# Performance work log

Hardware: AMD Instinct MI355X
Metric: run time of the kernel (lower is better)

The kernel has to match this reference:

```python
import jax, jax.numpy as jnp
import numpy as np
import math


def _interp_linear(x, t_out):
    # x: [B, D, Lin] -> [B, D, t_out]; matches torch F.interpolate(mode='linear', align_corners=False)
    lin = x.shape[-1]
    pos = (jnp.arange(t_out, dtype=jnp.float32) + 0.5) * (lin / t_out) - 0.5
    pos = jnp.clip(pos, 0.0, lin - 1.0)
    lo = jnp.floor(pos).astype(jnp.int32)
    hi = jnp.minimum(lo + 1, lin - 1)
    w = pos - lo.astype(jnp.float32)
    return x[..., lo] * (1.0 - w) + x[..., hi] * w


def _forward(x, in_w, in_b, gq_w, gq_b, gk_w, gk_b, gv_w, gv_b, go_w, go_b, curv,
             wav0, wav1, wav2, wav3, wrec_w, wrec_b,
             te1_w, te1_b, te2_w, te2_b, td1_w, td1_b, td2_w, td2_b, bd_w, bd_b,
             cc_w, cc_b, ln_g, ln_b, mm1_w, mm1_b, mm2_w, mm2_b,
             dn1_w, dn1_b, dn2_w, dn2_b, dn3_w, dn3_b, out_w, out_b,
             noise_sched, noise):
    B, T, _ = x.shape
    L, H = curv.shape
    D = in_w.shape[1]
    hd = D // H
    dn = ('NCH', 'OIH', 'NCH')
    h = x @ in_w + in_b
    total_loss = jnp.float32(0.0)
    wavs = [wav0, wav1, wav2, wav3]
    for l in range(L):  # static small layer loop
        # ---- GeometricAttention (vectorized hyperbolic-distance softmax) ----
        q = (h @ gq_w[l] + gq_b[l]).reshape(B, T, H, hd)
        k = (h @ gk_w[l] + gk_b[l]).reshape(B, T, H, hd)
        v = (h @ gv_w[l] + gv_b[l]).reshape(B, T, H, hd)
        c = jnp.abs(curv[l]) + 1e-8                       # [H]
        cb = c[None, :, None, None]
        qn = jnp.einsum('bthd,bthd->bht', q, q)           # [B,H,T]
        kn = jnp.einsum('bthd,bthd->bht', k, k)
        qk = jnp.einsum('bihd,bjhd->bhij', q, k)          # [B,H,T,T]
        d2 = jnp.maximum(qn[:, :, :, None] + kn[:, :, None, :] - 2.0 * qk, 0.0)
        denom = jnp.maximum((1.0 - cb * qn[:, :, :, None]) * (1.0 - cb * kn[:, :, None, :]), 1e-5)
        arg = jnp.maximum(1.0 + cb * (2.0 * d2) / denom, 1.00001)
        dist = jnp.arccosh(arg) / jnp.sqrt(cb)
        attn = jax.nn.softmax(-dist, axis=-1)             # temperature = 1.0
        geom = jnp.einsum('bhij,bjhd->bihd', attn, v).reshape(B, T, D) @ go_w[l] + go_b[l]
        # ---- WaveletTransform ----
        xf = h.transpose(0, 2, 1)                          # [B,D,T]
        decomps = []
        for i, wv in enumerate(wavs):
            filt = jax.nn.softmax(wv[l], axis=-1)          # [D,K]
            K = filt.shape[-1]
            dec = jax.lax.conv_general_dilated(xf, filt[:, None, :], (1,), [(K - 1, 0)],
                                               feature_group_count=D, dimension_numbers=dn)
            dec = dec[:, :, ::2 ** (i + 1)]
            decomps.append(_interp_linear(dec, T))
        comb = jnp.concatenate(decomps, axis=1).transpose(0, 2, 1)  # [B,T,4D]
        wave = comb @ wrec_w[l] + wrec_b[l]
        # ---- TopologicalLayer ----
        tf = jax.nn.relu(h @ te1_w[l] + te1_b[l]) @ te2_w[l] + te2_b[l]
        topo = h + (jax.nn.relu(tf @ td1_w[l] + td1_b[l]) @ td2_w[l] + td2_b[l])
        bd = tf @ bd_w[l] + bd_b[l]
        total_loss = total_loss + jnp.mean(jax.nn.relu(bd[..., 0] - bd[..., 1] + 0.1))
        # ---- CausalConvolution (kernel 3, dilation 2**l) ----
        dil = 2 ** l
        pad = 2 * dil
        cc = jax.lax.conv_general_dilated(h.transpose(0, 2, 1), cc_w[l], (1,), [(pad, 0)],
                                          rhs_dilation=(dil,), dimension_numbers=dn)
        cc = (cc + cc_b[l][None, :, None]).transpose(0, 2, 1)
        # ---- combine + LayerNorm (dropout is identity in eval) ----
        s = geom + wave + topo + cc
        mu = jnp.mean(s, axis=-1, keepdims=True)
        var = jnp.var(s, axis=-1, keepdims=True)
        h = (s - mu) / jnp.sqrt(var + 1e-5) * ln_g + ln_b
    # ---- manifold mixer (T > 1 branch) ----
    last = h[:, -1]
    pen = h[:, -2]
    mix = jnp.tanh(jnp.concatenate([last, pen], axis=-1) @ mm1_w + mm1_b) @ mm2_w + mm2_b
    cur = last + mix
    # ---- diffusion refinement ----
    half = D // 2
    emb_f = jnp.exp(jnp.arange(half, dtype=jnp.float32) * (-math.log(10000.0) / (half - 1)))
    S = noise.shape[0]
    for t in range(S):  # static diffusion_steps=10
        noisy = cur + noise[t] * noise_sched[t]
        te = jnp.full((B, 1), float(t), dtype=jnp.float32) * emb_f[None, :]
        temb = jnp.concatenate([jnp.sin(te), jnp.cos(te)], axis=-1)  # [B,D]
        di = jnp.concatenate([noisy, temb], axis=-1)
        npred = jax.nn.silu(jax.nn.silu(di @ dn1_w + dn1_b) @ dn2_w + dn2_b) @ dn3_w + dn3_b
        cur = cur - npred * noise_sched[t]
    pred = cur @ out_w + out_b
    return pred, total_loss


def setup_inputs() -> dict:
    key = jax.random.key(0)
    B, T, Din, D, L, H, P, S = 16, 256, 384, 512, 6, 8, 64, 10
    ctr = [0]
    def rn(shape, s=0.05):
        ctr[0] += 1
        return jax.random.normal(jax.random.fold_in(key, ctr[0]), shape, jnp.float32) * s
    d = {}
    d['x'] = rn((B, T, Din), 1.0)
    d['in_w'] = rn((Din, D)); d['in_b'] = rn((D,), 0.01)
    for nm in ['gq', 'gk', 'gv', 'go']:
        d[nm + '_w'] = rn((L, D, D)); d[nm + '_b'] = rn((L, D), 0.01)
    d['curv'] = rn((L, H), 1.0)
    for i in range(4):
        d['wav%d' % i] = rn((L, D, 2 ** (i + 2)), 1.0)
    d['wrec_w'] = rn((L, 4 * D, D)); d['wrec_b'] = rn((L, D), 0.01)
    d['te1_w'] = rn((L, D, P)); d['te1_b'] = rn((L, P), 0.01)
    d['te2_w'] = rn((L, P, P)); d['te2_b'] = rn((L, P), 0.01)
    d['td1_w'] = rn((L, P, D)); d['td1_b'] = rn((L, D), 0.01)
    d['td2_w'] = rn((L, D, D)); d['td2_b'] = rn((L, D), 0.01)
    d['bd_w'] = rn((L, P, 2)); d['bd_b'] = rn((L, 2), 0.01)
    d['cc_w'] = rn((L, D, D, 3)); d['cc_b'] = rn((L, D), 0.01)
    d['ln_g'] = jnp.ones((D,), jnp.float32); d['ln_b'] = jnp.zeros((D,), jnp.float32)
    d['mm1_w'] = rn((2 * D, D)); d['mm1_b'] = rn((D,), 0.01)
    d['mm2_w'] = rn((D, D)); d['mm2_b'] = rn((D,), 0.01)
    d['dn1_w'] = rn((2 * D, D)); d['dn1_b'] = rn((D,), 0.01)
    d['dn2_w'] = rn((D, D)); d['dn2_b'] = rn((D,), 0.01)
    d['dn3_w'] = rn((D, D)); d['dn3_b'] = rn((D,), 0.01)
    d['out_w'] = rn((D, Din)); d['out_b'] = rn((Din,), 0.01)
    d['noise_sched'] = jnp.linspace(0.1, 0.9, S).astype(jnp.float32)
    d['noise'] = rn((S, B, D), 1.0)
    return d


def reference(x, in_w, in_b, gq_w, gq_b, gk_w, gk_b, gv_w, gv_b, go_w, go_b, curv,
              wav0, wav1, wav2, wav3, wrec_w, wrec_b,
              te1_w, te1_b, te2_w, te2_b, td1_w, td1_b, td2_w, td2_b, bd_w, bd_b,
              cc_w, cc_b, ln_g, ln_b, mm1_w, mm1_b, mm2_w, mm2_b,
              dn1_w, dn1_b, dn2_w, dn2_b, dn3_w, dn3_b, out_w, out_b,
              noise_sched, noise):
    return _forward(x, in_w, in_b, gq_w, gq_b, gk_w, gk_b, gv_w, gv_b, go_w, go_b, curv,
                    wav0, wav1, wav2, wav3, wrec_w, wrec_b,
                    te1_w, te1_b, te2_w, te2_b, td1_w, td1_b, td2_w, td2_b, bd_w, bd_b,
                    cc_w, cc_b, ln_g, ln_b, mm1_w, mm1_b, mm2_w, mm2_b,
                    dn1_w, dn1_b, dn2_w, dn2_b, dn3_w, dn3_b, out_w, out_b,
                    noise_sched, noise)
```

## Files before the change

kernel.cpp:

```cpp
#include <hip/hip_runtime.h>
#include <hip/hip_bf16.h>
#include <math.h>

#define BB 16
#define TT 256
#define DIN 384
#define DD 512
#define LL 6
#define HH 8
#define PP 64
#define SS 10
#define BT (BB*TT)

enum { ACT_NONE=0, ACT_RELU=1, ACT_TANH=2, ACT_SILU=3, ACT_RELU_TAIL=4 };

typedef __attribute__((ext_vector_type(8))) short bf16x8;
typedef __attribute__((ext_vector_type(4))) float f32x4;
typedef __hip_bfloat16 bh16;

typedef const __attribute__((address_space(1))) void gvoid_t;
typedef __attribute__((address_space(3))) void lvoid_t;
__device__ __forceinline__ void gload16(const void* g, void* l) {
    __builtin_amdgcn_global_load_lds((gvoid_t*)g, (lvoid_t*)l, 16, 0, 0);
}
// ... 91 lines not shown
                    acc[fm][fn] = __builtin_amdgcn_mfma_f32_16x16x32_bf16(
                        a[fm][ks], b[fn][ks], acc[fm][fn], 0, 0, 0);
        __syncthreads();
    }

    #pragma unroll
    for (int fm = 0; fm < 4; ++fm) {
        #pragma unroll
        for (int fn = 0; fn < 2; ++fn) {
            int gc = col0 + wn*32 + fn*16 + (lane & 15);
            float bs = bias ? bias[gc] : 0.f;
            #pragma unroll
            for (int r = 0; r < 4; ++r) {
                int gr = row0 + wm*64 + fm*16 + (lane>>4)*4 + r;
                float v = acc[fm][fn][r] + bs;
                if (act == ACT_RELU) v = fmaxf(v, 0.f);
                else if (act == ACT_RELU_TAIL && gc >= 1536) v = fmaxf(v, 0.f);
                size_t o = (size_t)gr*ldc + gc;
                if (Cf) { if (accum) Cf[o] += v; else Cf[o] = v; }
                if (Cb) Cb[o] = __float2bfloat16(v);
            }
        }
    }
}

__global__ __launch_bounds__(256) void topo_kernel(
    const bh16* __restrict__ t1,
    const bh16* __restrict__ te2T,
    const float* __restrict__ te2b,
    const bh16* __restrict__ td1T,
    const float* __restrict__ td1b,
    const float* __restrict__ bdw, const float* __restrict__ bdb,
    float* __restrict__ loss,
    bh16* __restrict__ tdb)
{
    __shared__ bf16x8 As[128*8];
    __shared__ bf16x8 Bs[64*8];
    __shared__ float redT[2][128];
    __shared__ float bsumS;

    const int bx = blockIdx.x, by = blockIdx.y;
    const int lane = threadIdx.x & 63, w = threadIdx.x >> 6;
    const int wm = w >> 1, wn = w & 1;
    const int row0 = by * 128;

    #pragma unroll
    for (int j = 0; j < 4; ++j) {
        int c = ((w*4 + j) << 6) + lane;
        int row = c >> 3, chk = c & 7, schk = chk ^ (row & 7);
        gload16(t1 + (size_t)(row0 + row)*1600 + schk*8, &As[(w*4+j)*64]);
    }
    #pragma unroll
    for (int j = 0; j < 2; ++j) {
        int c = ((w*2 + j) << 6) + lane;
        int row = c >> 3, chk = c & 7, schk = chk ^ (row & 7);
        gload16(te2T + (size_t)row*64 + schk*8, &Bs[(w*2+j)*64]);
    }
    asm volatile("s_waitcnt vmcnt(0)" ::: "memory");
    __syncthreads();

    f32x4 acc[4][2];
    #pragma unroll
    for (int i = 0; i < 4; ++i)
        #pragma unroll
        for (int j = 0; j < 2; ++j) acc[i][j] = (f32x4){0.f,0.f,0.f,0.f};
    {
        bf16x8 a[4][2], b[2][2];
        #pragma unroll
        for (int fm = 0; fm < 4; ++fm) {
            int row = wm*64 + fm*16 + (lane & 15);
            #pragma unroll
            for (int ks = 0; ks < 2; ++ks)
                a[fm][ks] = As[row*8 + ((ks*4 + (lane>>4)) ^ (row & 7))];
        }
        #pragma unroll
        for (int fn = 0; fn < 2; ++fn) {
            int col = wn*32 + fn*16 + (lane & 15);
            #pragma unroll
            for (int ks = 0; ks < 2; ++ks)
                b[fn][ks] = Bs[col*8 + ((ks*4 + (lane>>4)) ^ (col & 7))];
        }
        #pragma unroll
        for (int ks = 0; ks < 2; ++ks)
            #pragma unroll
            for (int fm = 0; fm < 4; ++fm)
                #pragma unroll
                for (int fn = 0; fn < 2; ++fn)
                    acc[fm][fn] = __builtin_amdgcn_mfma_f32_16x16x32_bf16(
                        a[fm][ks], b[fn][ks], acc[fm][fn], 0, 0, 0);
    }
    #pragma unroll
    for (int fn = 0; fn < 2; ++fn) {
        int gc = wn*32 + fn*16 + (lane & 15);
        float bs = te2b[gc];
        #pragma unroll
        for (int fm = 0; fm < 4; ++fm)
            #pragma unroll
            for (int r = 0; r < 4; ++r) acc[fm][fn][r] += bs;
    }

    if (bx == 0) {
        float bconst = (bdb[0] - bdb[1]) + 0.1f;
        float wv[2];
        #pragma unroll
        for (int fn = 0; fn < 2; ++fn) {
            int gc = wn*32 + fn*16 + (lane & 15);
            wv[fn] = bdw[gc*2] - bdw[gc*2 + 1];
        }
        float dp[4][4];
        #pragma unroll
        for (int fm = 0; fm < 4; ++fm)
            #pragma unroll
            for (int r = 0; r < 4; ++r) {
                dp[fm][r] = acc[fm][0][r]*wv[0] + acc[fm][1][r]*wv[1];
                #pragma unroll
                for (int off = 1; off < 16; off <<= 1)
                    dp[fm][r] += __shfl_xor(dp[fm][r], off);
            }
        if ((lane & 15) == 0)
            #pragma unroll
            for (int fm = 0; fm < 4; ++fm)
                #pragma unroll
                for (int r = 0; r < 4; ++r)
                    redT[wn][wm*64 + fm*16 + (lane>>4)*4 + r] = dp[fm][r];
        if (threadIdx.x == 0) bsumS = 0.f;
        __syncthreads();
        if (wn == 0 && (lane & 15) == 0) {
            float ls = 0.f;
            #pragma unroll
            for (int fm = 0; fm < 4; ++fm)
                #pragma unroll
                for (int r = 0; r < 4; ++r) {
                    int rowl = wm*64 + fm*16 + (lane>>4)*4 + r;
                    ls += fmaxf(dp[fm][r] + redT[1][rowl] + bconst, 0.f);
                }
            atomicAdd(&bsumS, ls);
        }
        __syncthreads();
        if (threadIdx.x == 0) atomicAdd(loss, bsumS * (1.f / 4096.f));
    }

    __syncthreads();
    #pragma unroll
    for (int fm = 0; fm < 4; ++fm)
        #pragma unroll
        for (int fn = 0; fn < 2; ++fn)
            #pragma unroll
            for (int r = 0; r < 4; ++r) {
                int rowl = wm*64 + fm*16 + (lane>>4)*4 + r;
                int gc = wn*32 + fn*16 + (lane & 15);
                ((bh16*)As)[(rowl*8 + ((gc >> 3) ^ (rowl & 7)))*8 + (gc & 7)] =
                    __float2bfloat16(acc[fm][fn][r]);
            }
    #pragma unroll
    for (int j = 0; j < 2; ++j) {
        int c = ((w*2 + j) << 6) + lane;
        int row = c >> 3, chk = c & 7, schk = chk ^ (row & 7);
        gload16(td1T + (size_t)(bx*64 + row)*64 + schk*8, &Bs[(w*2+j)*64]);
    }
    asm volatile("s_waitcnt vmcnt(0)" ::: "memory");
    __syncthreads();

    f32x4 acc2[4][2];
    #pragma unroll
    for (int i = 0; i < 4; ++i)
        #pragma unroll
        for (int j = 0; j < 2; ++j) acc2[i][j] = (f32x4){0.f,0.f,0.f,0.f};
    {
        bf16x8 a[4][2], b[2][2];
        #pragma unroll
        for (int fm = 0; fm < 4; ++fm) {
            int row = wm*64 + fm*16 + (lane & 15);
            #pragma unroll
            for (int ks = 0; ks < 2; ++ks)
                a[fm][ks] = As[row*8 + ((ks*4 + (lane>>4)) ^ (row & 7))];
        }
        #pragma unroll
        for (int fn = 0; fn < 2; ++fn) {
            int col = wn*32 + fn*16 + (lane & 15);
            #pragma unroll
            for (int ks = 0; ks < 2; ++ks)
                b[fn][ks] = Bs[col*8 + ((ks*4 + (lane>>4)) ^ (col & 7))];
        }
        #pragma unroll
        for (int ks = 0; ks < 2; ++ks)
            #pragma unroll
            for (int fm = 0; fm < 4; ++fm)
                #pragma unroll
                for (int fn = 0; fn < 2; ++fn)
                    acc2[fm][fn] = __builtin_amdgcn_mfma_f32_16x16x32_bf16(
                        a[fm][ks], b[fn][ks], acc2[fm][fn], 0, 0, 0);
    }
    #pragma unroll
    for (int fm = 0; fm < 4; ++fm)
        #pragma unroll
        for (int fn = 0; fn < 2; ++fn) {
            int gcol = bx*64 + wn*32 + fn*16 + (lane & 15);
            float bs = td1b[gcol];
            #pragma unroll
            for (int r = 0; r < 4; ++r) {
                int gr = row0 + wm*64 + fm*16 + (lane>>4)*4 + r;
                tdb[(size_t)gr*512 + gcol] = __float2bfloat16(fmaxf(acc2[fm][fn][r] + bs, 0.f));
            }
        }
}

__global__ __launch_bounds__(256) void fattn_kernel(
    const bh16* __restrict__ qkv,
    const float* __restrict__ curv,
    bh16* __restrict__ gmb)
{
    __shared__ bf16x8 Qs[64*8];
    __shared__ bf16x8 Ks[256*8];
    __shared__ __align__(16) bh16 Ps[64*64];
    __shared__ bf16x8 Bv[64*8];
    __shared__ unsigned short Vst[64*72];
    __shared__ float redA[2][64];
    __shared__ float redB[2][64];
    __shared__ float qnS[64];
    __shared__ float knS[256];

    const int rh = blockIdx.x;
    const int bh = blockIdx.y;
    const int b = bh >> 3, hh = bh & 7;
    const int lane = threadIdx.x & 63, w = threadIdx.x >> 6;
    const int wm = w >> 1, wn = w & 1;

// ... 210 lines not shown
                vb[fn][ks] = Bv[col*8 + ((ks*4 + (lane>>4)) ^ (col & 7))];
        }
        #pragma unroll
        for (int ks = 0; ks < 2; ++ks)
            #pragma unroll
            for (int fm = 0; fm < 2; ++fm)
                #pragma unroll
                for (int fn = 0; fn < 2; ++fn)
                    acc2[fm][fn] = __builtin_amdgcn_mfma_f32_16x16x32_bf16(
                        pa[fm][ks], vb[fn][ks], acc2[fm][fn], 0, 0, 0);
    }

    #pragma unroll
    for (int fm = 0; fm < 2; ++fm)
        #pragma unroll
        for (int fn = 0; fn < 2; ++fn)
            #pragma unroll
            for (int r = 0; r < 4; ++r) {
                int rowl = wm*32 + fm*16 + (lane>>4)*4 + r;
                int col = wn*32 + fn*16 + (lane & 15);
                gmb[((size_t)(b*256 + rh*64 + rowl))*512 + hh*64 + col] =
                    __float2bfloat16(acc2[fm][fn][r]);
            }
}

__global__ __launch_bounds__(256) void fgemm_kernel(
    const bh16* __restrict__ A0, const bh16* __restrict__ A1,
    const bh16* __restrict__ A2, const bh16* __restrict__ A3,
    const bh16* __restrict__ B0, const bh16* __restrict__ B1,
    const bh16* __restrict__ B2, const bh16* __restrict__ B3,
    const float* __restrict__ bias,
    float* __restrict__ Cf0, float* __restrict__ Cf1,
    float* __restrict__ Cf2, float* __restrict__ Cf3,
    int dil, const bh16* __restrict__ zp)
{
    __shared__ bf16x8 As[128*8];
    __shared__ bf16x8 Bs[64*8];

    int bx = blockIdx.x, by = blockIdx.y;
    xcd_swizzle_always(bx, by);
    const int zz = blockIdx.z;
    const int ktlo = zz * 18;
    const int kthi = ktlo + 18;

    const int tid  = threadIdx.x;
    const int lane = tid & 63, w = tid >> 6;
// ... 122 lines not shown
    const int col = col0 + ar;
    float bs = bias ? bias[col] : 0.f;
    float sc = scaleptr ? *scaleptr : 0.f;
    #pragma unroll
    for (int r = 0; r < 4; ++r) {
        int row = (lane >> 4) * 4 + r;
        float v = acc[r] + bs;
        if (pre) v += pre[(size_t)row * N + col];
        if (act == ACT_SILU)      v = v / (1.f + expf(-v));
        else if (act == ACT_TANH) v = tanhf(v);
        if (curf) {
            size_t o = (size_t)row * 512 + col;
            float nc = curf[o] - v * sc;
            curf[o] = nc;
            curb[o] = __float2bfloat16(nc);
        } else {
            size_t o = (size_t)z * oZ + (size_t)row * N + col;
            if (Of) Of[o] = v;
            if (Ob) Ob[o] = __float2bfloat16(v);
        }
    }
}

__device__ __forceinline__ f32x4 lslice(const unsigned short* A, int lda, const bh16* Bt, int ldb,
                                        int col0, int K, int lane)
{
    const int ar = lane & 15;
    const int koff = (lane >> 4) * 8;
    const unsigned short* arow = A + (size_t)ar * lda + koff;
    const bh16* brow = Bt + (size_t)(col0 + ar) * ldb + koff;
    f32x4 acc = {0.f, 0.f, 0.f, 0.f};
    const int nkt = K >> 5;
    for (int kt0 = 0; kt0 < nkt; kt0 += 8) {
        bf16x8 av[8], bv[8];
        #pragma unroll
        for (int j = 0; j < 8; ++j) {
            av[j] = *(const bf16x8*)(arow + (size_t)(kt0 + j) * 32);
            bv[j] = *(const bf16x8*)(brow + (size_t)(kt0 + j) * 32);
        }
        #pragma unroll
        for (int j = 0; j < 8; ++j)
            acc = __builtin_amdgcn_mfma_f32_16x16x32_bf16(av[j], bv[j], acc, 0, 0, 0);
    }
    return acc;
}

__device__ __forceinline__ void st_store(unsigned* st, int row, int colr, int lane, float v)
{
    float other = __shfl_xor(v, 1);
    if (!(lane & 1)) {
        unsigned lo = (unsigned)__bfloat16_as_ushort(__float2bfloat16(v));
        unsigned hi = (unsigned)__bfloat16_as_ushort(__float2bfloat16(other));
        __hip_atomic_store(st + ((row * 512 + colr) >> 1), lo | (hi << 16),
                           __ATOMIC_RELAXED, __HIP_MEMORY_SCOPE_AGENT);
    }
}

__device__ __forceinline__ void st_stage(unsigned short* ALds, const unsigned* st, int tid)
{
    for (int e = tid; e < 4096; e += 256) {
        unsigned uv = __hip_atomic_load(st + e, __ATOMIC_RELAXED, __HIP_MEMORY_SCOPE_AGENT);
        int row = e >> 8, cp = (e & 255) << 1;
        *(unsigned*)(ALds + row * 520 + cp) = uv;
    }
    __syncthreads();
}

__device__ __forceinline__ void gridbar(int* ctr, int* bar)
{
    __syncthreads();
    if (threadIdx.x == 0) {
        *bar += 8;
        __hip_atomic_fetch_add(ctr, 1, __ATOMIC_RELAXED, __HIP_MEMORY_SCOPE_AGENT);
        while (__hip_atomic_load(ctr, __ATOMIC_RELAXED, __HIP_MEMORY_SCOPE_AGENT) < *bar)
            __builtin_amdgcn_s_sleep(1);
    }
    __syncthreads();
}

__global__ __launch_bounds__(256) void head2_kernel(
    const float* __restrict__ h,
    const bh16* __restrict__ mm1T, const float* __restrict__ mm1b,
    const bh16* __restrict__ mm2T, const float* __restrict__ mm2b,
    const bh16* __restrict__ dn1T,
    const bh16* __restrict__ dn2T, const float* __restrict__ dn2b,
    const bh16* __restrict__ dn3T, const float* __restrict__ dn3b,
    const bh16* __restrict__ outT, const float* __restrict__ outb,
    const float* __restrict__ pre1, const float* __restrict__ nsched,
    unsigned* __restrict__ stTM, unsigned* __restrict__ stCur,
    unsigned* __restrict__ stD1, unsigned* __restrict__ stD2,
    float* __restrict__ out, int* __restrict__ ctr)
{
    __shared__ __align__(16) unsigned short catL[16 * 1032];
    __shared__ __align__(16) unsigned short ALds[16 * 520];
    const int bx = blockIdx.x;
    const int tid = threadIdx.x;
    const int lane = tid & 63, w = tid >> 6;
    int bar = 0;
    const int col0 = bx * 64 + w * 16;
    const int colr = col0 + (lane & 15);
    const int row0 = (lane >> 4) * 4;

    for (int e = tid; e < 16 * 1024; e += 256) {
        int k = e & 1023, b = e >> 10;
        float v = (k < 512) ? h[((size_t)b * TT + 255) * DD + k]
                            : h[((size_t)b * TT + 254) * DD + (k - 512)];
        catL[b * 1032 + k] = __bfloat16_as_ushort(__float2bfloat16(v));
    }
    __syncthreads();

    {
        f32x4 acc = lslice(catL, 1032, mm1T, 1024, col0, 1024, lane);
        float bs = mm1b[colr];
        #pragma unroll
        for (int r = 0; r < 4; ++r)
            st_store(stTM, row0 + r, colr, lane, tanhf(acc[r] + bs));
    }
    gridbar(ctr, &bar);

    float cur_reg[4];
    {
        st_stage(ALds, stTM, tid);
        f32x4 acc = lslice(ALds, 520, mm2T, 512, col0, 512, lane);
        float bs = mm2b[colr];
        #pragma unroll
        for (int r = 0; r < 4; ++r) {
            float cv = h[((size_t)(row0 + r) * TT + 255) * DD + colr] + acc[r] + bs;
            cur_reg[r] = cv;
            st_store(stCur, row0 + r, colr, lane, cv);
        }
    }
    gridbar(ctr, &bar);

    for (int t = 0; t < SS; ++t) {
        float sc = nsched[t];
        {
            st_stage(ALds, stCur, tid);
            f32x4 acc = lslice(ALds, 520, dn1T, 1024, col0, 512, lane);
            #pragma unroll
            for (int r = 0; r < 4; ++r) {
                float v = acc[r] + pre1[(size_t)t * 8192 + (row0 + r) * 512 + colr];
                v = v / (1.f + expf(-v));
                st_store(stD1, row0 + r, colr, lane, v);
            }
        }
        gridbar(ctr, &bar);
        {
            st_stage(ALds, stD1, tid);
            f32x4 acc = lslice(ALds, 520, dn2T, 512, col0, 512, lane);
            float bs = dn2b[colr];
            #pragma unroll
            for (int r = 0; r < 4; ++r) {
                float v = acc[r] + bs;
                v = v / (1.f + expf(-v));
                st_store(stD2, row0 + r, colr, lane, v);
            }
        }
        gridbar(ctr, &bar);
        {
            st_stage(ALds, stD2, tid);
            f32x4 acc = lslice(ALds, 520, dn3T, 512, col0, 512, lane);
            float bs = dn3b[colr];
            #pragma unroll
            for (int r = 0; r < 4; ++r) {
                float nc = cur_reg[r] - (acc[r] + bs) * sc;
                cur_reg[r] = nc;
                st_store(stCur, row0 + r, colr, lane, nc);
            }
        }
        gridbar(ctr, &bar);
    }

    {
        st_stage(ALds, stCur, tid);
        if (bx < 6) {
            f32x4 acc = lslice(ALds, 520, outT, 512, col0, 512, lane);
            float bs = outb[colr];
            #pragma unroll
            for (int r = 0; r < 4; ++r)
                out[(size_t)(row0 + r) * 384 + colr] = acc[r] + bs;
        }
    }
}

__global__ __launch_bounds__(256) void wave4_kernel(const bh16* __restrict__ hb,
                                                    const float* __restrict__ wav0,
                                                    const float* __restrict__ wav1,
                                                    const float* __restrict__ wav2,
                                                    const float* __restrict__ wav3,
                                                    int l,
                                                    bh16* __restrict__ comb)
{
    __shared__ float dtile[66 * 64];
    __shared__ float ftile[32 * 64];
    const int dblk = blockIdx.x;
    const int iy = blockIdx.y;
    const int b = blockIdx.z;
    const int i = iy >> 1, thalf = iy & 1;
    const int Karr[4] = {4, 8, 16, 32};
    const int K = Karr[i], sv = 2 << i, Ti = 128 >> i;
    const int tid = threadIdx.x;
    const int dbase = dblk * 64;
    if (tid < 64) {
        const float* wsrc = (i == 0) ? wav0 : (i == 1) ? wav1 : (i == 2) ? wav2 : wav3;
        const float* row = wsrc + ((size_t)l * DD + dbase + tid) * K;
        float mx = -1e30f;
        for (int k = 0; k < K; ++k) mx = fmaxf(mx, row[k]);
        float s = 0.f;
        for (int k = 0; k < K; ++k) { float e = expf(row[k] - mx); ftile[k*64 + tid] = e; s += e; }
        float inv = 1.f / s;
        for (int k = 0; k < K; ++k) ftile[k*64 + tid] *= inv;
    }
    const float invsv = 1.f / (float)sv;
    const int t0 = thalf * 128;
    float p0 = ((float)t0 + 0.5f) * invsv - 0.5f;
    p0 = fminf(fmaxf(p0, 0.f), (float)(Ti - 1));
    const int jbase = (int)p0;
    float p1 = ((float)(t0 + 127) + 0.5f) * invsv - 0.5f;
    p1 = fminf(fmaxf(p1, 0.f), (float)(Ti - 1));
    const int him = min((int)p1 + 1, Ti - 1);
    const int jcount = him - jbase + 1;
    __syncthreads();
    const bh16* hcol = hb + (size_t)b * (TT * DD) + dbase;
    for (int e = tid; e < jcount * 64; e += 256) {
        int jl = e >> 6, d0 = e & 63;
        int j = jbase + jl;
        int tb = j * sv - (K - 1);
        float acc = 0.f;
        #pragma unroll 4
        for (int k = 0; k < K; ++k) {
            int t = tb + k;
            if (t >= 0)
                acc += b2f(*(const unsigned short*)(hcol + (size_t)t * DD + d0)) * ftile[k * 64 + d0];
        }
        dtile[jl * 64 + d0] = acc;
    }
    __syncthreads();
    for (int e = tid; e < 128 * 64; e += 256) {
        int tl = e >> 6, d0 = e & 63;
        int t = t0 + tl;
        float pos = ((float)t + 0.5f) * invsv - 0.5f;
        pos = fminf(fmaxf(pos, 0.f), (float)(Ti - 1));
        int lo = (int)pos;
        int hi = min(lo + 1, Ti - 1);
        float w = pos - (float)lo;
        float v = dtile[(lo - jbase) * 64 + d0] * (1.f - w) + dtile[(hi - jbase) * 64 + d0] * w;
        comb[((size_t)b * TT + t) * 2048 + i * 512 + dbase + d0] = __float2bfloat16(v);
    }
}

__global__ __launch_bounds__(256) void add_ln_kernel(const float* __restrict__ s0, const float* __restrict__ s1,
                                                     const float* __restrict__ s2, const float* __restrict__ s3,
                                                     float* __restrict__ h, bh16* __restrict__ hb,
                                                     const float* __restrict__ g, const float* __restrict__ be)
{
    int lane = threadIdx.x & 63, wid = threadIdx.x >> 6;
    size_t row = (size_t)blockIdx.x * 4 + wid;
    const float* sr0 = s0 + row * DD;
    const float* sr1 = s1 + row * DD;
    const float* sr2 = s2 + row * DD;
    const float* sr3 = s3 + row * DD;
    float* hr = h + row * DD;
    bh16* hbr = hb + row * DD;
    float xv[8]; float sum = 0.f;
    #pragma unroll
    for (int u = 0; u < 8; ++u) {
        int c = lane + u * 64;
        xv[u] = sr0[c] + sr1[c] + sr2[c] + sr3[c] + hr[c];
        sum += xv[u];
    }
// ... 198 lines not shown
    const float* ln_g   = (const float*)d_in[30];
    const float* ln_b   = (const float*)d_in[31];
    const float* mm1_w  = (const float*)d_in[32];
    const float* mm1_b  = (const float*)d_in[33];
    const float* mm2_w  = (const float*)d_in[34];
    const float* mm2_b  = (const float*)d_in[35];
    const float* dn1_w  = (const float*)d_in[36];
    const float* dn1_b  = (const float*)d_in[37];
    const float* dn2_w  = (const float*)d_in[38];
    const float* dn2_b  = (const float*)d_in[39];
    const float* dn3_w  = (const float*)d_in[40];
    const float* dn3_b  = (const float*)d_in[41];
    const float* out_w  = (const float*)d_in[42];
    const float* out_b  = (const float*)d_in[43];
    const float* nsched = (const float*)d_in[44];
    const float* noise  = (const float*)d_in[45];
    float* out = (float*)d_out;
    float* ws  = (float*)d_ws;

    const size_t o_h   = 0;
    const size_t o_dec = 2097152;
    const size_t o_s   = 4194304;
    const size_t o_at  = 6619136;
    const size_t o_cur = 15046656;
    const size_t o_qkb = 15054848;
    const size_t o_bs  = 15064448;
    const size_t o_ctr = 15067520;
    const size_t FP32_TOTAL = 15095808;
    const size_t b_xb   = 0;
    const size_t b_hb   = 1572864;
    const size_t b_qkv  = 3670016;
    const size_t b_pb   = 12320768;
    const size_t b_gmb  = 20709376;
    const size_t b_tdb  = 22806528;
    const size_t b_zp   = 25165824;
    const size_t b_inwT = 25166336;
    const size_t b_qkvT = 25362944;
    const size_t b_goT  = 30278144;
    const size_t b_wrT  = 31851008;
    const size_t b_td1T = 38142464;
    const size_t b_td2T = 38339072;
    const size_t b_te2T = 39911936;
    const size_t b_ccT  = 39936512;
    const size_t BF16_TOTAL = 44655104;
    const size_t TOTAL_BYTES = FP32_TOTAL * 4 + BF16_TOTAL * 2;
    if (ws_size < TOTAL_BYTES) { fail_kernel<<<1, 1, 0, stream>>>(out); return; }

// ... 44 lines not shown
        mgemm_kernel<<<g, 256, 0, stream>>>(A, lda, Bt, ldb, bias, Cf, Cb, ldc, N, K,
                                            shift, accum, act, zp);
    };

    init_kernel<<<1, 128, 0, stream>>>(zp, out + BB * DIN, ctr);
    convx_kernel<<<BT * DIN / 256, 256, 0, stream>>>(x, xb);
    wtrans_kernel<<<dim3(DD/32, DIN/32, 1), 256, 0, stream>>>(in_w, inwT, DIN, DD, (long)DIN*DD);
    wtrans4_kernel<<<dim3(50, 16, 6), 256, 0, stream>>>(gq_w, gk_w, gv_w, te1_w, qkvT);
    qkvbias_kernel<<<38, 256, 0, stream>>>(gq_b, gk_b, gv_b, te1_b, qkvbias,
                                           go_b, wrec_b, td2_b, cc_b, bsum);
    wtrans_kernel<<<dim3(16, 16, 6), 256, 0, stream>>>(go_w, goT, DD, DD, (long)DD*DD);
    wtrans_kernel<<<dim3(16, 64, 6), 256, 0, stream>>>(wrec_w, wrT, 2048, DD, 2048L*DD);
    wtrans_kernel<<<dim3(16, 2, 6), 256, 0, stream>>>(td1_w, td1T, PP, DD, (long)PP*DD);
    wtrans_kernel<<<dim3(16, 16, 6), 256, 0, stream>>>(td2_w, td2T, DD, DD, (long)DD*DD);
    wtrans_kernel<<<dim3(2, 2, 6), 256, 0, stream>>>(te2_w, te2T, PP, PP, (long)PP*PP);
    ccconv_kernel<<<18432, 256, 0, stream>>>(cc_w, ccT);

    mgp(xb, DIN, inwT, DIN, in_b, h_, hb, DD, BT, DD, DIN, 0, 0, ACT_NONE);

    for (int l = 0; l < LL; ++l) {
        mgp(hb, DD, qkvT + (size_t)l*819200, DD, qkvbias + (size_t)l*1600,
            nullptr, qkvb, 1600, BT, 1600, DD, 0, 0, ACT_RELU_TAIL);
        fattn_kernel<<<dim3(4, 128), 256, 0, stream>>>(qkvb, curv + (size_t)l*HH, gmb);
        wave4_kernel<<<dim3(8, 8, 16), 256, 0, stream>>>(hb, wav0, wav1, wav2, wav3, l, combb);
        topo_kernel<<<dim3(8, 32), 256, 0, stream>>>(
            qkvb + 1536, te2T + (size_t)l*4096, te2_b + (size_t)l*PP,
            td1T + (size_t)l*32768, td1_b + (size_t)l*DD,
            bd_w + (size_t)l*PP*2, bd_b + (size_t)l*2, out + BB*DIN, tdb);
        fgemm_kernel<<<dim3(8, 32, 4), 256, 0, stream>>>(
            gmb, combb, tdb, hb,
            goT + (size_t)l*262144, wrT + (size_t)l*1048576,
            td2T + (size_t)l*262144, ccT + (size_t)l*786432,
            bsum + (size_t)l*512, s_, s2_, s3_, s4_, 1 << l, zp);
        add_ln_kernel<<<BT/4, 256, 0, stream>>>(s_, s2_, s3_, s4_, h_, hb, ln_g, ln_b);
    }

    wtransH_kernel<<<1984, 256, 0, stream>>>(mm1_w, mm2_w, dn1_w, dn2_w, dn3_w, out_w,
                                             mm1T, mm2T, dn1T, dn2T, dn3T, outT);
    build_E_kernel<<<640, 256, 0, stream>>>(noise, nsched, E16);
    hgemm16_kernel<<<dim3(8, 1, SS), 256, 0, stream>>>(
        E16, 1024, 16*1024, dn1T, 1024, dn1_b, nullptr, pre1, nullptr, 8192,
        512, 1024, ACT_NONE, nullptr, nullptr, nullptr);
    head2_kernel<<<8, 256, 0, stream>>>(
        h_, mm1T, mm1_b, mm2T, mm2_b, dn1T, dn2T, dn2_b, dn3T, dn3_b,
        outT, out_b, pre1, nsched, stTM, stCur, stD1, stD2, out, ctr);
}
```

Before: 1.003 ms.

## Merge wavelet and topology kernels; prefetch head weights across grid barriers

Combines the wavelet-decomposition and topology MLP kernels into one launch that dispatches on block index, with a union of their shared-memory layouts. This removes one launch per layer and lets the two independent jobs share the GPU. In the sequential head kernel, each next-stage weight slice is loaded into registers before the grid barrier so the load overlaps the wait. The state staging is also widened to 64-bit atomic loads. The cost is more register pressure from holding 16 bf16x8 vectors per lane and a larger fused kernel.

Measured after the change: 1.009 ms. About the same (+0.6%).

```diff
diff --git a/kernel.cpp b/kernel.cpp
--- a/kernel.cpp
+++ b/kernel.cpp
@@ -137,187 +137,6 @@
             }
         }
     }
-}
-
-__global__ __launch_bounds__(256) void topo_kernel(
-    const bh16* __restrict__ t1,
-    const bh16* __restrict__ te2T,
-    const float* __restrict__ te2b,
-    const bh16* __restrict__ td1T,
-    const float* __restrict__ td1b,
-    const float* __restrict__ bdw, const float* __restrict__ bdb,
-    float* __restrict__ loss,
-    bh16* __restrict__ tdb)
-{
-    __shared__ bf16x8 As[128*8];
-    __shared__ bf16x8 Bs[64*8];
-    __shared__ float redT[2][128];
-    __shared__ float bsumS;
-
-    const int bx = blockIdx.x, by = blockIdx.y;
-    const int lane = threadIdx.x & 63, w = threadIdx.x >> 6;
-    const int wm = w >> 1, wn = w & 1;
-    const int row0 = by * 128;
-
-    #pragma unroll
-    for (int j = 0; j < 4; ++j) {
-        int c = ((w*4 + j) << 6) + lane;
-        int row = c >> 3, chk = c & 7, schk = chk ^ (row & 7);
-        gload16(t1 + (size_t)(row0 + row)*1600 + schk*8, &As[(w*4+j)*64]);
-    }
-    #pragma unroll
-    for (int j = 0; j < 2; ++j) {
-        int c = ((w*2 + j) << 6) + lane;
-        int row = c >> 3, chk = c & 7, schk = chk ^ (row & 7);
-        gload16(te2T + (size_t)row*64 + schk*8, &Bs[(w*2+j)*64]);
-    }
-    asm volatile("s_waitcnt vmcnt(0)" ::: "memory");
-    __syncthreads();
-
-    f32x4 acc[4][2];
-    #pragma unroll
-    for (int i = 0; i < 4; ++i)
-        #pragma unroll
-        for (int j = 0; j < 2; ++j) acc[i][j] = (f32x4){0.f,0.f,0.f,0.f};
-    {
-        bf16x8 a[4][2], b[2][2];
-        #pragma unroll
-        for (int fm = 0; fm < 4; ++fm) {
-            int row = wm*64 + fm*16 + (lane & 15);
-            #pragma unroll
-            for (int ks = 0; ks < 2; ++ks)
-                a[fm][ks] = As[row*8 + ((ks*4 + (lane>>4)) ^ (row & 7))];
-        }
-        #pragma unroll
-        for (int fn = 0; fn < 2; ++fn) {
-            int col = wn*32 + fn*16 + (lane & 15);
-            #pragma unroll
-            for (int ks = 0; ks < 2; ++ks)
-                b[fn][ks] = Bs[col*8 + ((ks*4 + (lane>>4)) ^ (col & 7))];
-        }
-        #pragma unroll
-        for (int ks = 0; ks < 2; ++ks)
-            #pragma unroll
-            for (int fm = 0; fm < 4; ++fm)
-                #pragma unroll
-                for (int fn = 0; fn < 2; ++fn)
-                    acc[fm][fn] = __builtin_amdgcn_mfma_f32_16x16x32_bf16(
-                        a[fm][ks], b[fn][ks], acc[fm][fn], 0, 0, 0);
-    }
-    #pragma unroll
-    for (int fn = 0; fn < 2; ++fn) {
-        int gc = wn*32 + fn*16 + (lane & 15);
-        float bs = te2b[gc];
-        #pragma unroll
-        for (int fm = 0; fm < 4; ++fm)
-            #pragma unroll
-            for (int r = 0; r < 4; ++r) acc[fm][fn][r] += bs;
-    }
-
-    if (bx == 0) {
-        float bconst = (bdb[0] - bdb[1]) + 0.1f;
-        float wv[2];
-        #pragma unroll
-        for (int fn = 0; fn < 2; ++fn) {
-            int gc = wn*32 + fn*16 + (lane & 15);
-            wv[fn] = bdw[gc*2] - bdw[gc*2 + 1];
-        }
-        float dp[4][4];
-        #pragma unroll
-        for (int fm = 0; fm < 4; ++fm)
-            #pragma unroll
-            for (int r = 0; r < 4; ++r) {
-                dp[fm][r] = acc[fm][0][r]*wv[0] + acc[fm][1][r]*wv[1];
-                #pragma unroll
-                for (int off = 1; off < 16; off <<= 1)
-                    dp[fm][r] += __shfl_xor(dp[fm][r], off);
-            }
-        if ((lane & 15) == 0)
-            #pragma unroll
-            for (int fm = 0; fm < 4; ++fm)
-                #pragma unroll
-                for (int r = 0; r < 4; ++r)
-                    redT[wn][wm*64 + fm*16 + (lane>>4)*4 + r] = dp[fm][r];
-        if (threadIdx.x == 0) bsumS = 0.f;
-        __syncthreads();
-        if (wn == 0 && (lane & 15) == 0) {
-            float ls = 0.f;
-            #pragma unroll
-            for (int fm = 0; fm < 4; ++fm)
-                #pragma unroll
-                for (int r = 0; r < 4; ++r) {
-                    int rowl = wm*64 + fm*16 + (lane>>4)*4 + r;
-                    ls += fmaxf(dp[fm][r] + redT[1][rowl] + bconst, 0.f);
-                }
-            atomicAdd(&bsumS, ls);
-        }
-        __syncthreads();
-        if (threadIdx.x == 0) atomicAdd(loss, bsumS * (1.f / 4096.f));
-    }
-
-    __syncthreads();
-    #pragma unroll
-    for (int fm = 0; fm < 4; ++fm)
-        #pragma unroll
-        for (int fn = 0; fn < 2; ++fn)
-            #pragma unroll
-            for (int r = 0; r < 4; ++r) {
-                int rowl = wm*64 + fm*16 + (lane>>4)*4 + r;
-                int gc = wn*32 + fn*16 + (lane & 15);
-                ((bh16*)As)[(rowl*8 + ((gc >> 3) ^ (rowl & 7)))*8 + (gc & 7)] =
-                    __float2bfloat16(acc[fm][fn][r]);
-            }
-    #pragma unroll
-    for (int j = 0; j < 2; ++j) {
-        int c = ((w*2 + j) << 6) + lane;
-        int row = c >> 3, chk = c & 7, schk = chk ^ (row & 7);
-        gload16(td1T + (size_t)(bx*64 + row)*64 + schk*8, &Bs[(w*2+j)*64]);
-    }
-    asm volatile("s_waitcnt vmcnt(0)" ::: "memory");
-    __syncthreads();
-
-    f32x4 acc2[4][2];
-    #pragma unroll
-    for (int i = 0; i < 4; ++i)
-        #pragma unroll
-        for (int j = 0; j < 2; ++j) acc2[i][j] = (f32x4){0.f,0.f,0.f,0.f};
-    {
-        bf16x8 a[4][2], b[2][2];
-        #pragma unroll
-        for (int fm = 0; fm < 4; ++fm) {
-            int row = wm*64 + fm*16 + (lane & 15);
-            #pragma unroll
-            for (int ks = 0; ks < 2; ++ks)
-                a[fm][ks] = As[row*8 + ((ks*4 + (lane>>4)) ^ (row & 7))];
-        }
-        #pragma unroll
-        for (int fn = 0; fn < 2; ++fn) {
-            int col = wn*32 + fn*16 + (lane & 15);
-            #pragma unroll
-            for (int ks = 0; ks < 2; ++ks)
-                b[fn][ks] = Bs[col*8 + ((ks*4 + (lane>>4)) ^ (col & 7))];
-        }
-        #pragma unroll
-        for (int ks = 0; ks < 2; ++ks)
-            #pragma unroll
-            for (int fm = 0; fm < 4; ++fm)
-                #pragma unroll
-                for (int fn = 0; fn < 2; ++fn)
-                    acc2[fm][fn] = __builtin_amdgcn_mfma_f32_16x16x32_bf16(
-                        a[fm][ks], b[fn][ks], acc2[fm][fn], 0, 0, 0);
-    }
-    #pragma unroll
-    for (int fm = 0; fm < 4; ++fm)
-        #pragma unroll
-        for (int fn = 0; fn < 2; ++fn) {
-            int gcol = bx*64 + wn*32 + fn*16 + (lane & 15);
-            float bs = td1b[gcol];
-            #pragma unroll
-            for (int r = 0; r < 4; ++r) {
-                int gr = row0 + wm*64 + fm*16 + (lane>>4)*4 + r;
-                tdb[(size_t)gr*512 + gcol] = __float2bfloat16(fmaxf(acc2[fm][fn][r] + bs, 0.f));
-            }
-        }
 }
 
 __global__ __launch_bounds__(256) void fattn_kernel(
@@ -574,6 +393,254 @@
                 gmb[((size_t)(b*256 + rh*64 + rowl))*512 + hh*64 + col] =
                     __float2bfloat16(acc2[fm][fn][r]);
             }
+}
+
+union WTSmem {
+    struct { float dtile[66*64]; float ftile[32*64]; } wv;
+    struct { bf16x8 As[128*8]; bf16x8 Bs[64*8]; float redT[2][128]; float bsumS; } tp;
+};
+
+__global__ __launch_bounds__(256) void midwt_kernel(
+    const bh16* __restrict__ hb,
+    const float* __restrict__ wav0, const float* __restrict__ wav1,
+    const float* __restrict__ wav2, const float* __restrict__ wav3,
+    int l, bh16* __restrict__ comb,
+    const bh16* __restrict__ t1,
+    const bh16* __restrict__ te2T, const float* __restrict__ te2b,
+    const bh16* __restrict__ td1T, const float* __restrict__ td1b,
+    const float* __restrict__ bdw, const float* __restrict__ bdb,
+    float* __restrict__ loss, bh16* __restrict__ tdb)
+{
+    __shared__ WTSmem sm;
+    const int bid = blockIdx.x;
+    const int tid = threadIdx.x;
+
+    if (bid < 1024) {
+        float* dtile = sm.wv.dtile;
+        float* ftile = sm.wv.ftile;
+        const int dblk = bid & 7;
+        const int iy = (bid >> 3) & 7;
+        const int b = bid >> 6;
+        const int i = iy >> 1, thalf = iy & 1;
+        const int Karr[4] = {4, 8, 16, 32};
+        const int K = Karr[i], sv = 2 << i, Ti = 128 >> i;
+        const int dbase = dblk * 64;
+        if (tid < 64) {
+            const float* wsrc = (i == 0) ? wav0 : (i == 1) ? wav1 : (i == 2) ? wav2 : wav3;
+            const float* row = wsrc + ((size_t)l * DD + dbase + tid) * K;
+            float mx = -1e30f;
+            for (int k = 0; k < K; ++k) mx = fmaxf(mx, row[k]);
+            float s = 0.f;
+            for (int k = 0; k < K; ++k) { float e = expf(row[k] - mx); ftile[k*64 + tid] = e; s += e; }
+            float inv = 1.f / s;
+            for (int k = 0; k < K; ++k) ftile[k*64 + tid] *= inv;
+        }
+        const float invsv = 1.f / (float)sv;
+        const int t0 = thalf * 128;
+        float p0 = ((float)t0 + 0.5f) * invsv - 0.5f;
+        p0 = fminf(fmaxf(p0, 0.f), (float)(Ti - 1));
+        const int jbase = (int)p0;
+        float p1 = ((float)(t0 + 127) + 0.5f) * invsv - 0.5f;
+        p1 = fminf(fmaxf(p1, 0.f), (float)(Ti - 1));
+        const int him = min((int)p1 + 1, Ti - 1);
+        const int jcount = him - jbase + 1;
+        __syncthreads();
+        const bh16* hcol = hb + (size_t)b * (TT * DD) + dbase;
+        for (int e = tid; e < jcount * 64; e += 256) {
+            int jl = e >> 6, d0 = e & 63;
+            int j = jbase + jl;
+            int tb = j * sv - (K - 1);
+            float acc = 0.f;
+            #pragma unroll 4
+            for (int k = 0; k < K; ++k) {
+                int t = tb + k;
+                if (t >= 0)
+                    acc += b2f(*(const unsigned short*)(hcol + (size_t)t * DD + d0)) * ftile[k * 64 + d0];
+            }
+            dtile[jl * 64 + d0] = acc;
+        }
+        __syncthreads();
+        for (int e = tid; e < 128 * 64; e += 256) {
+            int tl = e >> 6, d0 = e & 63;
+            int t = t0 + tl;
+            float pos = ((float)t + 0.5f) * invsv - 0.5f;
+            pos = fminf(fmaxf(pos, 0.f), (float)(Ti - 1));
+            int lo = (int)pos;
+            int hi = min(lo + 1, Ti - 1);
+            float w = pos - (float)lo;
+            float v = dtile[(lo - jbase) * 64 + d0] * (1.f - w) + dtile[(hi - jbase) * 64 + d0] * w;
+            comb[((size_t)b * TT + t) * 2048 + i * 512 + dbase + d0] = __float2bfloat16(v);
+        }
+        return;
+    }
+
+    bf16x8* As = sm.tp.As;
+    bf16x8* Bs = sm.tp.Bs;
+    const int lid = bid - 1024;
+    const int bx = lid & 7, by = lid >> 3;
+    const int lane = tid & 63, w = tid >> 6;
+    const int wm = w >> 1, wn = w & 1;
+    const int row0 = by * 128;
+
+    #pragma unroll
+    for (int j = 0; j < 4; ++j) {
+        int c = ((w*4 + j) << 6) + lane;
+        int row = c >> 3, chk = c & 7, schk = chk ^ (row & 7);
+        gload16(t1 + (size_t)(row0 + row)*1600 + schk*8, &As[(w*4+j)*64]);
+    }
+    #pragma unroll
+    for (int j = 0; j < 2; ++j) {
+        int c = ((w*2 + j) << 6) + lane;
+        int row = c >> 3, chk = c & 7, schk = chk ^ (row & 7);
+        gload16(te2T + (size_t)row*64 + schk*8, &Bs[(w*2+j)*64]);
+    }
+    asm volatile("s_waitcnt vmcnt(0)" ::: "memory");
+    __syncthreads();
+
+    f32x4 acc[4][2];
+    #pragma unroll
+    for (int i = 0; i < 4; ++i)
+        #pragma unroll
+        for (int j = 0; j < 2; ++j) acc[i][j] = (f32x4){0.f,0.f,0.f,0.f};
+    {
+        bf16x8 a[4][2], b[2][2];
+        #pragma unroll
+        for (int fm = 0; fm < 4; ++fm) {
+            int row = wm*64 + fm*16 + (lane & 15);
+            #pragma unroll
+            for (int ks = 0; ks < 2; ++ks)
+                a[fm][ks] = As[row*8 + ((ks*4 + (lane>>4)) ^ (row & 7))];
+        }
+        #pragma unroll
+        for (int fn = 0; fn < 2; ++fn) {
+            int col = wn*32 + fn*16 + (lane & 15);
+            #pragma unroll
+            for (int ks = 0; ks < 2; ++ks)
+                b[fn][ks] = Bs[col*8 + ((ks*4 + (lane>>4)) ^ (col & 7))];
+        }
+        #pragma unroll
+        for (int ks = 0; ks < 2; ++ks)
+            #pragma unroll
+            for (int fm = 0; fm < 4; ++fm)
+                #pragma unroll
+                for (int fn = 0; fn < 2; ++fn)
+                    acc[fm][fn] = __builtin_amdgcn_mfma_f32_16x16x32_bf16(
+                        a[fm][ks], b[fn][ks], acc[fm][fn], 0, 0, 0);
+    }
+    #pragma unroll
+    for (int fn = 0; fn < 2; ++fn) {
+        int gc = wn*32 + fn*16 + (lane & 15);
+        float bs = te2b[gc];
+        #pragma unroll
+        for (int fm = 0; fm < 4; ++fm)
+            #pragma unroll
+            for (int r = 0; r < 4; ++r) acc[fm][fn][r] += bs;
+    }
+
+    if (bx == 0) {
+        float bconst = (bdb[0] - bdb[1]) + 0.1f;
+        float wv[2];
+        #pragma unroll
+        for (int fn = 0; fn < 2; ++fn) {
+            int gc = wn*32 + fn*16 + (lane & 15);
+            wv[fn] = bdw[gc*2] - bdw[gc*2 + 1];
+        }
+        float dp[4][4];
+        #pragma unroll
+        for (int fm = 0; fm < 4; ++fm)
+            #pragma unroll
+            for (int r = 0; r < 4; ++r) {
+                dp[fm][r] = acc[fm][0][r]*wv[0] + acc[fm][1][r]*wv[1];
+                #pragma unroll
+                for (int off = 1; off < 16; off <<= 1)
+                    dp[fm][r] += __shfl_xor(dp[fm][r], off);
+            }
+        if ((lane & 15) == 0)
+            #pragma unroll
+            for (int fm = 0; fm < 4; ++fm)
+                #pragma unroll
+                for (int r = 0; r < 4; ++r)
+                    sm.tp.redT[wn][wm*64 + fm*16 + (lane>>4)*4 + r] = dp[fm][r];
+        if (tid == 0) sm.tp.bsumS = 0.f;
+        __syncthreads();
+        if (wn == 0 && (lane & 15) == 0) {
+            float ls = 0.f;
+            #pragma unroll
+            for (int fm = 0; fm < 4; ++fm)
+                #pragma unroll
+                for (int r = 0; r < 4; ++r) {
+                    int rowl = wm*64 + fm*16 + (lane>>4)*4 + r;
+                    ls += fmaxf(dp[fm][r] + sm.tp.redT[1][rowl] + bconst, 0.f);
+                }
+            atomicAdd(&sm.tp.bsumS, ls);
+        }
+        __syncthreads();
+        if (tid == 0) atomicAdd(loss, sm.tp.bsumS * (1.f / 4096.f));
+    }
+
+    __syncthreads();
+    #pragma unroll
+    for (int fm = 0; fm < 4; ++fm)
+        #pragma unroll
+        for (int fn = 0; fn < 2; ++fn)
+            #pragma unroll
+            for (int r = 0; r < 4; ++r) {
+                int rowl = wm*64 + fm*16 + (lane>>4)*4 + r;
+                int gc = wn*32 + fn*16 + (lane & 15);
+                ((bh16*)As)[(rowl*8 + ((gc >> 3) ^ (rowl & 7)))*8 + (gc & 7)] =
+                    __float2bfloat16(acc[fm][fn][r]);
+            }
+    #pragma unroll
+    for (int j = 0; j < 2; ++j) {
+        int c = ((w*2 + j) << 6) + lane;
+        int row = c >> 3, chk = c & 7, schk = chk ^ (row & 7);
+        gload16(td1T + (size_t)(bx*64 + row)*64 + schk*8, &Bs[(w*2+j)*64]);
+    }
+    asm volatile("s_waitcnt vmcnt(0)" ::: "memory");
+    __syncthreads();
+
+    f32x4 acc2[4][2];
+    #pragma unroll
+    for (int i = 0; i < 4; ++i)
+        #pragma unroll
+        for (int j = 0; j < 2; ++j) acc2[i][j] = (f32x4){0.f,0.f,0.f,0.f};
+    {
+        bf16x8 a[4][2], b[2][2];
+        #pragma unroll
+        for (int fm = 0; fm < 4; ++fm) {
+            int row = wm*64 + fm*16 + (lane & 15);
+            #pragma unroll
+            for (int ks = 0; ks < 2; ++ks)
+                a[fm][ks] = As[row*8 + ((ks*4 + (lane>>4)) ^ (row & 7))];
+        }
+        #pragma unroll
+        for (int fn = 0; fn < 2; ++fn) {
+            int col = wn*32 + fn*16 + (lane & 15);
+            #pragma unroll
+            for (int ks = 0; ks < 2; ++ks)
+                b[fn][ks] = Bs[col*8 + ((ks*4 + (lane>>4)) ^ (col & 7))];
+        }
+        #pragma unroll
+        for (int ks = 0; ks < 2; ++ks)
+            #pragma unroll
+            for (int fm = 0; fm < 4; ++fm)
+                #pragma unroll
+                for (int fn = 0; fn < 2; ++fn)
+                    acc2[fm][fn] = __builtin_amdgcn_mfma_f32_16x16x32_bf16(
+                        a[fm][ks], b[fn][ks], acc2[fm][fn], 0, 0, 0);
+    }
+    #pragma unroll
+    for (int fm = 0; fm < 4; ++fm)
+        #pragma unroll
+        for (int fn = 0; fn < 2; ++fn) {
+            int gcol = bx*64 + wn*32 + fn*16 + (lane & 15);
+            float bs = td1b[gcol];
+            #pragma unroll
+            for (int r = 0; r < 4; ++r) {
+                int gr = row0 + wm*64 + fm*16 + (lane>>4)*4 + r;
+                tdb[(size_t)gr*512 + gcol] = __float2bfloat16(fmaxf(acc2[fm][fn][r] + bs, 0.f));
+            }
+        }
 }
 
 __global__ __launch_bounds__(256) void fgemm_kernel(
@@ -742,6 +809,30 @@
     }
 }
 
+__device__ __forceinline__ void bload512(const bh16* Bt, int ldb, int col0, int lane, bf16x8 bv[16])
+{
+    const int ar = lane & 15;
+    const int koff = (lane >> 4) * 8;
+    const bh16* brow = Bt + (size_t)(col0 + ar) * ldb + koff;
+    #pragma unroll
+    for (int j = 0; j < 16; ++j)
+        bv[j] = *(const bf16x8*)(brow + (size_t)j * 32);
+}
+
+__device__ __forceinline__ f32x4 lmfma512(const unsigned short* A, int lda, int lane, const bf16x8 bv[16])
+{
+    const int ar = lane & 15;
+    const int koff = (lane >> 4) * 8;
+    const unsigned short* arow = A + (size_t)ar * lda + koff;
+    f32x4 acc = {0.f, 0.f, 0.f, 0.f};
+    #pragma unroll
+    for (int j = 0; j < 16; ++j) {
+        bf16x8 av = *(const bf16x8*)(arow + (size_t)j * 32);
+        acc = __builtin_amdgcn_mfma_f32_16x16x32_bf16(av, bv[j], acc, 0, 0, 0);
+    }
+    return acc;
+}
+
 __device__ __forceinline__ f32x4 lslice(const unsigned short* A, int lda, const bh16* Bt, int ldb,
                                         int col0, int K, int lane)
 {
@@ -778,10 +869,11 @@
 
 __device__ __forceinline__ void st_stage(unsigned short* ALds, const unsigned* st, int tid)
 {
-    for (int e = tid; e < 4096; e += 256) {
-        unsigned uv = __hip_atomic_load(st + e, __ATOMIC_RELAXED, __HIP_MEMORY_SCOPE_AGENT);
-        int row = e >> 8, cp = (e & 255) << 1;
-        *(unsigned*)(ALds + row * 520 + cp) = uv;
+    const unsigned long long* st64 = (const unsigned long long*)st;
+    for (int e = tid; e < 2048; e += 256) {
+        unsigned long long uv = __hip_atomic_load(st64 + e, __ATOMIC_RELAXED, __HIP_MEMORY_SCOPE_AGENT);
+        int row = e >> 7, cp = (e & 127) << 2;
+        *(unsigned long long*)(ALds + row * 520 + cp) = uv;
     }
     __syncthreads();
 }
@@ -798,7 +890,7 @@
     __syncthreads();
 }
 
-__global__ __launch_bounds__(256) void head2_kernel(
+__global__ __launch_bounds__(256) void head3_kernel(
     const float* __restrict__ h,
     const bh16* __restrict__ mm1T, const float* __restrict__ mm1b,
     const bh16* __restrict__ mm2T, const float* __restrict__ mm2b,
@@ -820,6 +912,7 @@
     const int col0 = bx * 64 + w * 16;
     const int colr = col0 + (lane & 15);
     const int row0 = (lane >> 4) * 4;
+    bf16x8 bv[16];
 
     for (int e = tid; e < 16 * 1024; e += 256) {
         int k = e & 1023, b = e >> 10;
@@ -836,12 +929,13 @@
         for (int r = 0; r < 4; ++r)
             st_store(stTM, row0 + r, colr, lane, tanhf(acc[r] + bs));
     }
+    bload512(mm2T, 512, col0, lane, bv);
     gridbar(ctr, &bar);
 
     float cur_reg[4];
     {
         st_stage(ALds, stTM, tid);
-        f32x4 acc = lslice(ALds, 520, mm2T, 512, col0, 512, lane);
+        f32x4 acc = lmfma512(ALds, 520, lane, bv);
         float bs = mm2b[colr];
         #pragma unroll
         for (int r = 0; r < 4; ++r) {
@@ -850,13 +944,14 @@
             st_store(stCur, row0 + r, colr, lane, cv);
         }
     }
+    bload512(dn1T, 1024, col0, lane, bv);
     gridbar(ctr, &bar);
 
     for (int t = 0; t < SS; ++t) {
         float sc = nsched[t];
         {
             st_stage(ALds, stCur, tid);
-            f32x4 acc = lslice(ALds, 520, dn1T, 1024, col0, 512, lane);
+            f32x4 acc = lmfma512(ALds, 520, lane, bv);
             #pragma unroll
             for (int r = 0; r < 4; ++r) {
                 float v = acc[r] + pre1[(size_t)t * 8192 + (row0 + r) * 512 + colr];
@@ -864,10 +959,11 @@
                 st_store(stD1, row0 + r, colr, lane, v);
             }
         }
+        bload512(dn2T, 512, col0, lane, bv);
         gridbar(ctr, &bar);
         {
             st_stage(ALds, stD1, tid);
-            f32x4 acc = lslice(ALds, 520, dn2T, 512, col0, 512, lane);
+            f32x4 acc = lmfma512(ALds, 520, lane, bv);
             float bs = dn2b[colr];
             #pragma unroll
             for (int r = 0; r < 4; ++r) {
@@ -876,10 +972,11 @@
                 st_store(stD2, row0 + r, colr, lane, v);
             }
         }
+        bload512(dn3T, 512, col0, lane, bv);
         gridbar(ctr, &bar);
         {
             st_stage(ALds, stD2, tid);
-            f32x4 acc = lslice(ALds, 520, dn3T, 512, col0, 512, lane);
+            f32x4 acc = lmfma512(ALds, 520, lane, bv);
             float bs = dn3b[colr];
             #pragma unroll
             for (int r = 0; r < 4; ++r) {
@@ -888,84 +985,20 @@
                 st_store(stCur, row0 + r, colr, lane, nc);
             }
         }
+        if (t < SS - 1) bload512(dn1T, 1024, col0, lane, bv);
+        else if (bx < 6) bload512(outT, 512, col0, lane, bv);
         gridbar(ctr, &bar);
     }
 
     {
         st_stage(ALds, stCur, tid);
         if (bx < 6) {
-            f32x4 acc = lslice(ALds, 520, outT, 512, col0, 512, lane);
+            f32x4 acc = lmfma512(ALds, 520, lane, bv);
             float bs = outb[colr];
             #pragma unroll
             for (int r = 0; r < 4; ++r)
                 out[(size_t)(row0 + r) * 384 + colr] = acc[r] + bs;
         }
-    }
-}
-
-__global__ __launch_bounds__(256) void wave4_kernel(const bh16* __restrict__ hb,
-                                                    const float* __restrict__ wav0,
-                                                    const float* __restrict__ wav1,
-                                                    const float* __restrict__ wav2,
-                                                    const float* __restrict__ wav3,
-                                                    int l,
-                                                    bh16* __restrict__ comb)
-{
-    __shared__ float dtile[66 * 64];
-    __shared__ float ftile[32 * 64];
-    const int dblk = blockIdx.x;
-    const int iy = blockIdx.y;
-    const int b = blockIdx.z;
-    const int i = iy >> 1, thalf = iy & 1;
-    const int Karr[4] = {4, 8, 16, 32};
-    const int K = Karr[i], sv = 2 << i, Ti = 128 >> i;
-    const int tid = threadIdx.x;
-    const int dbase = dblk * 64;
-    if (tid < 64) {
-        const float* wsrc = (i == 0) ? wav0 : (i == 1) ? wav1 : (i == 2) ? wav2 : wav3;
-        const float* row = wsrc + ((size_t)l * DD + dbase + tid) * K;
-        float mx = -1e30f;
-        for (int k = 0; k < K; ++k) mx = fmaxf(mx, row[k]);
-        float s = 0.f;
-        for (int k = 0; k < K; ++k) { float e = expf(row[k] - mx); ftile[k*64 + tid] = e; s += e; }
-        float inv = 1.f / s;
-        for (int k = 0; k < K; ++k) ftile[k*64 + tid] *= inv;
-    }
-    const float invsv = 1.f / (float)sv;
-    const int t0 = thalf * 128;
-    float p0 = ((float)t0 + 0.5f) * invsv - 0.5f;
-    p0 = fminf(fmaxf(p0, 0.f), (float)(Ti - 1));
-    const int jbase = (int)p0;
-    float p1 = ((float)(t0 + 127) + 0.5f) * invsv - 0.5f;
-    p1 = fminf(fmaxf(p1, 0.f), (float)(Ti - 1));
-    const int him = min((int)p1 + 1, Ti - 1);
-    const int jcount = him - jbase + 1;
-    __syncthreads();
-    const bh16* hcol = hb + (size_t)b * (TT * DD) + dbase;
-    for (int e = tid; e < jcount * 64; e += 256) {
-        int jl = e >> 6, d0 = e & 63;
-        int j = jbase + jl;
-        int tb = j * sv - (K - 1);
-        float acc = 0.f;
-        #pragma unroll 4
-        for (int k = 0; k < K; ++k) {
-            int t = tb + k;
-            if (t >= 0)
-                acc += b2f(*(const unsigned short*)(hcol + (size_t)t * DD + d0)) * ftile[k * 64 + d0];
-        }
-        dtile[jl * 64 + d0] = acc;
-    }
-    __syncthreads();
-    for (int e = tid; e < 128 * 64; e += 256) {
-        int tl = e >> 6, d0 = e & 63;
-        int t = t0 + tl;
-        float pos = ((float)t + 0.5f) * invsv - 0.5f;
-        pos = fminf(fmaxf(pos, 0.f), (float)(Ti - 1));
-        int lo = (int)pos;
-        int hi = min(lo + 1, Ti - 1);
-        float w = pos - (float)lo;
-        float v = dtile[(lo - jbase) * 64 + d0] * (1.f - w) + dtile[(hi - jbase) * 64 + d0] * w;
-        comb[((size_t)b * TT + t) * 2048 + i * 512 + dbase + d0] = __float2bfloat16(v);
     }
 }
 
@@ -1210,7 +1243,6 @@
     const size_t o_dec = 2097152;
     const size_t o_s   = 4194304;
     const size_t o_at  = 6619136;
-    const size_t o_cur = 15046656;
     const size_t o_qkb = 15054848;
     const size_t o_bs  = 15064448;
     const size_t o_ctr = 15067520;
@@ -1301,8 +1333,8 @@
         mgp(hb, DD, qkvT + (size_t)l*819200, DD, qkvbias + (size_t)l*1600,
             nullptr, qkvb, 1600, BT, 1600, DD, 0, 0, ACT_RELU_TAIL);
         fattn_kernel<<<dim3(4, 128), 256, 0, stream>>>(qkvb, curv + (size_t)l*HH, gmb);
-        wave4_kernel<<<dim3(8, 8, 16), 256, 0, stream>>>(hb, wav0, wav1, wav2, wav3, l, combb);
-        topo_kernel<<<dim3(8, 32), 256, 0, stream>>>(
+        midwt_kernel<<<1280, 256, 0, stream>>>(
+            hb, wav0, wav1, wav2, wav3, l, combb,
             qkvb + 1536, te2T + (size_t)l*4096, te2_b + (size_t)l*PP,
             td1T + (size_t)l*32768, td1_b + (size_t)l*DD,
             bd_w + (size_t)l*PP*2, bd_b + (size_t)l*2, out + BB*DIN, tdb);
@@ -1320,7 +1352,7 @@
     hgemm16_kernel<<<dim3(8, 1, SS), 256, 0, stream>>>(
         E16, 1024, 16*1024, dn1T, 1024, dn1_b, nullptr, pre1, nullptr, 8192,
         512, 1024, ACT_NONE, nullptr, nullptr, nullptr);
-    head2_kernel<<<8, 256, 0, stream>>>(
+    head3_kernel<<<8, 256, 0, stream>>>(
         h_, mm1T, mm1_b, mm2T, mm2_b, dn1T, dn2T, dn2_b, dn3T, dn3_b,
         outT, out_b, pre1, nsched, stTM, stCur, stD1, stD2, out, ctr);
 }
```
